# Kernel optimization log

Measured on AMD Instinct MI355X. Metric: run time of the kernel, lower is better.

The kernel has to match this reference:

```python
import jax, jax.numpy as jnp
import numpy as np

B, T, DIM, HEADS = 4, 2048, 1024, 16
D_K = DIM // HEADS


def setup_inputs() -> dict:
    key = jax.random.key(0)
    ks = jax.random.split(key, 5)
    x = jax.random.normal(ks[0], (B, T, DIM), dtype=jnp.float32)
    # nn.Linear params: weight [out, in], bias [out]
    w_qkv = jax.random.normal(ks[1], (3 * DIM, DIM), dtype=jnp.float32) / np.sqrt(DIM)
    b_qkv = jax.random.normal(ks[2], (3 * DIM,), dtype=jnp.float32) * 0.02
    w_out = jax.random.normal(ks[3], (DIM, DIM), dtype=jnp.float32) / np.sqrt(DIM)
    b_out = jax.random.normal(ks[4], (DIM,), dtype=jnp.float32) * 0.02
    # causal mask, broadcast over batch and heads: [1, 1, T, T]
    mask = jnp.tril(jnp.ones((T, T), dtype=jnp.int32))[None, None]
    return {"x": x, "w_qkv": w_qkv, "b_qkv": b_qkv, "w_out": w_out, "b_out": b_out, "mask": mask}


def reference(x, w_qkv, b_qkv, w_out, b_out, mask):
    Bb, Tt, D = x.shape
    # fused QKV projection: [B,T,3D] -> [3,B,H,T,d_k]
    qkv = (x @ w_qkv.T + b_qkv).reshape(Bb, Tt, 3, HEADS, D_K).transpose(2, 0, 3, 1, 4)
    q, k, v = qkv[0], qkv[1], qkv[2]
    scores = jnp.einsum("bhqd,bhkd->bhqk", q, k) / jnp.sqrt(jnp.float32(D_K))
    scores = jnp.where(mask == 0, -jnp.inf, scores)
    attn = jax.nn.softmax(scores, axis=-1)  # [B,H,T,T]
    context = jnp.einsum("bhqk,bhkd->bhqd", attn, v)
    context = context.transpose(0, 2, 1, 3).reshape(Bb, Tt, D)
    return context @ w_out.T + b_out
```

## Files before the change

kernel.cpp:

```cpp
#include <hip/hip_runtime.h>

typedef unsigned short ushort_t;
typedef __bf16 bf16x8 __attribute__((ext_vector_type(8)));
typedef float f32x4 __attribute__((ext_vector_type(4)));

#define BB 4
#define TT 2048
#define DIMD 1024
#define NH 16
#define DK 64
#define MROWS (BB * TT)
#define NQKV (3 * DIMD)

__device__ __forceinline__ ushort_t f2b(float f) {
  __bf16 h = (__bf16)f;
  union { __bf16 h; ushort_t u; } c; c.h = h; return c.u;
}
__device__ __forceinline__ float fexp2(float x) {
  float r;
  asm("v_exp_f32 %0, %1" : "=v"(r) : "v"(x));
  return r;
}

__device__ __forceinline__ void gload_lds16(const void* g, void* l) {
  __builtin_amdgcn_global_load_lds(
      (const __attribute__((address_space(1))) void*)g,
      (__attribute__((address_space(3))) void*)l,
      16, 0, 0);
}

__global__ __launch_bounds__(256) void cast_f32_bf16(
    const float* __restrict__ in, ushort_t* __restrict__ out, int n)
{
  const int i = (blockIdx.x * 256 + threadIdx.x) * 8;
  if (i >= n) return;
  float4 a = *(const float4*)(in + i);
  float4 b = *(const float4*)(in + i + 4);
  ushort_t o[8];
  o[0] = f2b(a.x); o[1] = f2b(a.y); o[2] = f2b(a.z); o[3] = f2b(a.w);
  o[4] = f2b(b.x); o[5] = f2b(b.y); o[6] = f2b(b.z); o[7] = f2b(b.w);
  *(uint4*)(out + i) = *(const uint4*)o;
}

template <bool OUT_F32>
__global__ __launch_bounds__(512, 4) void gemm_bt_pipe(
    const ushort_t* __restrict__ A, const ushort_t* __restrict__ W,
    const float* __restrict__ bias, void* __restrict__ Cp,
    int M, int N, int K)
{
  __shared__ __align__(16) ushort_t As[3][128 * 32];
  __shared__ __align__(16) ushort_t Bs[3][256 * 32];

  const int tid = threadIdx.x;
  const int wave = tid >> 6, lane = tid & 63;
  const int x = blockIdx.x & 7, j = blockIdx.x >> 3;
  const int bm = (x << 3) | (j & 7);
  const int bn = j >> 3;
  const int row0 = bm << 7, col0 = bn << 8;
  const int wm = (wave >> 2) << 6;
  const int wn = (wave & 3) << 6;
  const int fr = lane & 15;
  const int g  = lane >> 4;
  const int g4 = g << 2;
  const int csw = (g ^ (fr >> 2)) << 3;

  const int srow = lane >> 2;
  const int scol = ((lane & 3) ^ ((lane >> 4) & 3)) << 3;
  const int lbase = wave << 9;

  const ushort_t* Ag  = A + (size_t)(row0 + (wave << 4) + srow) * K + scol;
  const ushort_t* Wg0 = W + (size_t)(col0 + (wave << 4) + srow) * K + scol;
  const ushort_t* Wg1 = Wg0 + (size_t)128 * K;

#define STAGE_P(kt, buf)                                                      \
  {                                                                           \
    const size_t _k = (size_t)(kt) << 5;                                      \
    gload_lds16(Ag + _k,  &As[buf][lbase]);                                   \
    gload_lds16(Wg0 + _k, &Bs[buf][lbase]);                                   \
    gload_lds16(Wg1 + _k, &Bs[buf][4096 + lbase]);                            \
  }

  const int NT = K >> 5;
  STAGE_P(0, 0);
  STAGE_P(1, 1);

  f32x4 acc[4][4] = {};
  int cr = 0, st = 2;

  for (int t = 0; t < NT; ++t) {
    if (t + 1 < NT) asm volatile("s_waitcnt vmcnt(3)" ::: "memory");
    else            asm volatile("s_waitcnt vmcnt(0)" ::: "memory");
    __builtin_amdgcn_s_barrier();

    const ushort_t* as_ = As[cr];
    const ushort_t* bs_ = Bs[cr];
    bf16x8 af0 = *(const bf16x8*)&as_[(wm +      fr) * 32 + csw];
    bf16x8 af1 = *(const bf16x8*)&as_[(wm + 16 + fr) * 32 + csw];
    bf16x8 bw0 = *(const bf16x8*)&bs_[(wn +      fr) * 32 + csw];
    bf16x8 bw1 = *(const bf16x8*)&bs_[(wn + 16 + fr) * 32 + csw];
    bf16x8 bw2 = *(const bf16x8*)&bs_[(wn + 32 + fr) * 32 + csw];
    bf16x8 bw3 = *(const bf16x8*)&bs_[(wn + 48 + fr) * 32 + csw];
    if (t + 2 < NT) STAGE_P(t + 2, st);
    asm volatile("s_waitcnt lgkmcnt(0)" ::: "memory");
    __builtin_amdgcn_sched_barrier(0);
    __builtin_amdgcn_s_setprio(1);
    acc[0][0] = __builtin_amdgcn_mfma_f32_16x16x32_bf16(af0, bw0, acc[0][0], 0, 0, 0);
    acc[0][1] = __builtin_amdgcn_mfma_f32_16x16x32_bf16(af0, bw1, acc[0][1], 0, 0, 0);
    acc[0][2] = __builtin_amdgcn_mfma_f32_16x16x32_bf16(af0, bw2, acc[0][2], 0, 0, 0);
    acc[0][3] = __builtin_amdgcn_mfma_f32_16x16x32_bf16(af0, bw3, acc[0][3], 0, 0, 0);
    acc[1][0] = __builtin_amdgcn_mfma_f32_16x16x32_bf16(af1, bw0, acc[1][0], 0, 0, 0);
    acc[1][1] = __builtin_amdgcn_mfma_f32_16x16x32_bf16(af1, bw1, acc[1][1], 0, 0, 0);
    acc[1][2] = __builtin_amdgcn_mfma_f32_16x16x32_bf16(af1, bw2, acc[1][2], 0, 0, 0);
    acc[1][3] = __builtin_amdgcn_mfma_f32_16x16x32_bf16(af1, bw3, acc[1][3], 0, 0, 0);
    __builtin_amdgcn_s_setprio(0);

    bf16x8 af2 = *(const bf16x8*)&as_[(wm + 32 + fr) * 32 + csw];
    bf16x8 af3 = *(const bf16x8*)&as_[(wm + 48 + fr) * 32 + csw];
    asm volatile("s_waitcnt lgkmcnt(0)" ::: "memory");
    __builtin_amdgcn_sched_barrier(0);
    __builtin_amdgcn_s_setprio(1);
    acc[2][0] = __builtin_amdgcn_mfma_f32_16x16x32_bf16(af2, bw0, acc[2][0], 0, 0, 0);
    acc[2][1] = __builtin_amdgcn_mfma_f32_16x16x32_bf16(af2, bw1, acc[2][1], 0, 0, 0);
    acc[2][2] = __builtin_amdgcn_mfma_f32_16x16x32_bf16(af2, bw2, acc[2][2], 0, 0, 0);
    acc[2][3] = __builtin_amdgcn_mfma_f32_16x16x32_bf16(af2, bw3, acc[2][3], 0, 0, 0);
    acc[3][0] = __builtin_amdgcn_mfma_f32_16x16x32_bf16(af3, bw0, acc[3][0], 0, 0, 0);
    acc[3][1] = __builtin_amdgcn_mfma_f32_16x16x32_bf16(af3, bw1, acc[3][1], 0, 0, 0);
    acc[3][2] = __builtin_amdgcn_mfma_f32_16x16x32_bf16(af3, bw2, acc[3][2], 0, 0, 0);
    acc[3][3] = __builtin_amdgcn_mfma_f32_16x16x32_bf16(af3, bw3, acc[3][3], 0, 0, 0);
    __builtin_amdgcn_s_setprio(0);

    ++cr; if (cr == 3) cr = 0;
    ++st; if (st == 3) st = 0;
  }
#undef STAGE_P

#pragma unroll
  for (int jj = 0; jj < 4; ++jj) {
    const int col = col0 + wn + (jj << 4) + fr;
    const float bv = bias[col];
#pragma unroll
    for (int i = 0; i < 4; ++i)
#pragma unroll
      for (int r = 0; r < 4; ++r) {
        const size_t row = (size_t)(row0 + wm + (i << 4) + g4 + r);
        if constexpr (OUT_F32)
          ((float*)Cp)[row * (size_t)N + col] = acc[i][jj][r] + bv;
        else
          ((ushort_t*)Cp)[row * (size_t)N + col] = f2b(acc[i][jj][r] + bv);
      }
  }
}

template <bool OUT_F32>
__global__ __launch_bounds__(256) void gemm_bt_bias(
    const ushort_t* __restrict__ A, const ushort_t* __restrict__ W,
    const float* __restrict__ bias, void* __restrict__ Cp,
    int M, int N, int K)
{
  __shared__ __align__(16) ushort_t As[128 * 32];
  __shared__ __align__(16) ushort_t Bs[128 * 32];

  const int tid = threadIdx.x;
  const int wave = tid >> 6, lane = tid & 63;
  const int tiles_n = N >> 7;
  const int bm = blockIdx.x / tiles_n, bn = blockIdx.x % tiles_n;
  const int row0 = bm << 7, col0 = bn << 7;
  const int wm = (wave >> 1) << 6;
  const int wn = (wave & 1) << 6;
  const int fr = lane & 15;
  const int fk = (lane >> 4) << 3;
  const int g4 = (lane >> 4) << 2;

  const int sr = lane >> 2;
  const int csw = fk ^ (((fr >> 1) & 3) << 3);

  f32x4 acc[4][4] = {};

  for (int k0 = 0; k0 < K; k0 += 32) {
    __syncthreads();
#pragma unroll
    for (int p = 0; p < 2; ++p) {
      const int e = (wave << 9) + (p << 11);
      const int r = (e >> 5) + sr;
      const int c = ((lane & 3) << 3) ^ (((r >> 1) & 3) << 3);
      gload_lds16(A + (size_t)(row0 + r) * K + (k0 + c), As + e);
      gload_lds16(W + (size_t)(col0 + r) * K + (k0 + c), Bs + e);
    }
    __syncthreads();

    bf16x8 af[4], bw[4];
#pragma unroll
    for (int i = 0; i < 4; ++i) {
      af[i] = *(const bf16x8*)&As[(wm + (i << 4) + fr) * 32 + csw];
      bw[i] = *(const bf16x8*)&Bs[(wn + (i << 4) + fr) * 32 + csw];
    }
#pragma unroll
    for (int mi = 0; mi < 4; ++mi)
#pragma unroll
      for (int ni = 0; ni < 4; ++ni)
        acc[mi][ni] = __builtin_amdgcn_mfma_f32_16x16x32_bf16(af[mi], bw[ni], acc[mi][ni], 0, 0, 0);
  }

#pragma unroll
  for (int ni = 0; ni < 4; ++ni) {
    const int col = col0 + wn + (ni << 4) + fr;
    const float bv = bias[col];
#pragma unroll
    for (int mi = 0; mi < 4; ++mi)
#pragma unroll
      for (int r = 0; r < 4; ++r) {
        const size_t row = (size_t)(row0 + wm + (mi << 4) + g4 + r);
        if constexpr (OUT_F32)
          ((float*)Cp)[row * (size_t)N + col] = acc[mi][ni][r] + bv;
        else
          ((ushort_t*)Cp)[row * (size_t)N + col] = f2b(acc[mi][ni][r] + bv);
      }
  }
}

#define C1 0.18033688011112042f
__global__ __launch_bounds__(256, 4) void attn_fused(
    const ushort_t* __restrict__ qkv, ushort_t* __restrict__ ctx)
{
  __shared__ __align__(16) ushort_t Ks[2][64 * 64];
  __shared__ __align__(16) ushort_t U[8192];
  ushort_t* const Vt = U;
  ushort_t* const Ps = U + 4096;
  ushort_t* const Qs = U;

  const int tid = threadIdx.x, wave = tid >> 6, lane = tid & 63;
  const int fr = lane & 15;
  const int g  = lane >> 4;
  const int fk = g << 3;
  const int g4 = g << 2;

  const int bid = blockIdx.x;
  const int bq  = (bid >> 3) & 15;
  const int G   = (bid & 7) | ((bid >> 7) << 3);
  const int h   = G & 15;
  const int b   = G >> 4;

  const int srl = lane >> 3;
  const int scc = ((lane & 7) ^ srl) << 3;
  const int vr  = tid >> 2;
  const int vc  = (tid & 3) << 4;
  const int rsw = (fr & 7) << 3;

  const ushort_t* Kg = qkv + (size_t)b * TT * NQKV + DIMD + h * DK;
  const ushort_t* Vg = qkv + (size_t)b * TT * NQKV + 2 * DIMD + h * DK;

#pragma unroll 1
  for (int t = 0; t < 2; ++t) {
    const int qt = t ? (31 - bq) : bq;
    const int ktmax = qt;
    const size_t qrow0 = (size_t)b * TT + (size_t)qt * 64;

    __syncthreads();

    const ushort_t* Qg = qkv + qrow0 * NQKV + h * DK;
    uint4 va = *(const uint4*)(Vg + (size_t)vr * NQKV + vc);
    uint4 vb = *(const uint4*)(Vg + (size_t)vr * NQKV + vc + 8);
#pragma unroll
    for (int p = 0; p < 2; ++p) {
      const int e  = (wave << 10) + (p << 9);
      const int rr = (e >> 6) + srl;
      gload_lds16(Qg + (size_t)rr * NQKV + scc, Qs + e);
      gload_lds16(Kg + (size_t)rr * NQKV + scc, Ks[0] + e);
    }
    asm volatile("s_waitcnt vmcnt(0)" ::: "memory");
    __syncthreads();

    bf16x8 aqr[2];
#pragma unroll
    for (int ks = 0; ks < 2; ++ks)
      aqr[ks] = *(const bf16x8*)&Qs[((wave << 4) + fr) * 64 + (((ks << 5) + fk) ^ rsw)];
    __syncthreads();

    const int qrow = (qt << 6) + (wave << 4) + fr;
    float mrow = -1e30f, lrow = 0.f;
    f32x4 oacc[4] = {};
    int cur = 0;

    for (int kt = 0; kt <= ktmax; ++kt) {
      {
        __align__(16) ushort_t tmp[16];
        *(uint4*)&tmp[0] = va;
        *(uint4*)&tmp[8] = vb;
#pragma unroll
        for (int jj = 0; jj < 16; ++jj) {
          const int d  = vc + jj;
          const int hh = (d & 7) ^ ((d >> 3) & 7);
          Vt[d * 64 + (vr ^ (hh << 3))] = tmp[jj];
        }
      }
      if (kt < ktmax) {
        const size_t krow = (size_t)(kt + 1) << 6;
#pragma unroll
        for (int p = 0; p < 2; ++p) {
          const int e  = (wave << 10) + (p << 9);
          const int rr = (e >> 6) + srl;
          gload_lds16(Kg + (krow + rr) * NQKV + scc, Ks[cur ^ 1] + e);
        }
        va = *(const uint4*)(Vg + (krow + vr) * NQKV + vc);
        vb = *(const uint4*)(Vg + (krow + vr) * NQKV + vc + 8);
      }
      asm volatile("s_waitcnt lgkmcnt(0)" ::: "memory");
      __builtin_amdgcn_s_barrier();

      f32x4 s[4] = {};
      __builtin_amdgcn_s_setprio(1);
#pragma unroll
      for (int ks = 0; ks < 2; ++ks)
#pragma unroll
        for (int ni = 0; ni < 4; ++ni) {
          const bf16x8 bk = *(const bf16x8*)&Ks[cur][((ni << 4) + fr) * 64 + (((ks << 5) + fk) ^ rsw)];
          s[ni] = __builtin_amdgcn_mfma_f32_16x16x32_bf16(bk, aqr[ks], s[ni], 0, 0, 0);
        }
      __builtin_amdgcn_s_setprio(0);

      if (kt == ktmax) {
        const int kb = kt << 6;
#pragma unroll
        for (int ni = 0; ni < 4; ++ni)
#pragma unroll
          for (int r = 0; r < 4; ++r) {
            const int kc = kb + (ni << 4) + g4 + r;
            if (kc > qrow) s[ni][r] = -1e30f;
          }
      }

      float rm = -1e30f;
#pragma unroll
      for (int ni = 0; ni < 4; ++ni) {
        const float m01 = fmaxf(s[ni][0], s[ni][1]);
        const float m23 = fmaxf(s[ni][2], s[ni][3]);
        rm = fmaxf(rm, fmaxf(m01, m23));
      }
      rm = fmaxf(rm, __shfl_xor(rm, 16, 64));
      rm = fmaxf(rm, __shfl_xor(rm, 32, 64));

      if (__any(rm > mrow + 64.f)) {
        const float mn = fmaxf(mrow, rm);
        const float corr = fexp2((mrow - mn) * C1);
        mrow = mn;
        lrow *= corr;
#pragma unroll
        for (int ni = 0; ni < 4; ++ni) oacc[ni] *= corr;
      }
      const float nm2 = -mrow * C1;
      float rs = 0.f;
#pragma unroll
      for (int ni = 0; ni < 4; ++ni)
#pragma unroll
        for (int r = 0; r < 4; ++r) {
          const float pe = fexp2(fmaf(s[ni][r], C1, nm2));
          s[ni][r] = pe;
          rs += pe;
        }
      rs += __shfl_xor(rs, 16, 64);
      rs += __shfl_xor(rs, 32, 64);
      lrow += rs;

#pragma unroll
      for (int ni = 0; ni < 4; ++ni) {
        ushort_t o4[4];
#pragma unroll
        for (int r = 0; r < 4; ++r) o4[r] = f2b(s[ni][r]);
        *(uint2*)&Ps[(wave << 10) + fr * 64 + (((ni << 4) + g4) ^ rsw)] = *(const uint2*)o4;
      }
      asm volatile("s_waitcnt lgkmcnt(0)" ::: "memory");
      __builtin_amdgcn_sched_barrier(0);

      __builtin_amdgcn_s_setprio(1);
#pragma unroll
      for (int ks = 0; ks < 2; ++ks) {
        const bf16x8 ap = *(const bf16x8*)&Ps[(wave << 10) + fr * 64 + (((ks << 5) + fk) ^ rsw)];
#pragma unroll
        for (int ni = 0; ni < 4; ++ni) {
          const int hh = (fr & 7) ^ ((2 * ni + (fr >> 3)) & 7);
          const bf16x8 bv = *(const bf16x8*)&Vt[((ni << 4) + fr) * 64 + (((ks << 5) + fk) ^ (hh << 3))];
          oacc[ni] = __builtin_amdgcn_mfma_f32_16x16x32_bf16(bv, ap, oacc[ni], 0, 0, 0);
        }
      }
      __builtin_amdgcn_s_setprio(0);

      if (kt < ktmax) {
        asm volatile("s_waitcnt vmcnt(0)" ::: "memory");
        __syncthreads();
      }
      cur ^= 1;
    }

    const float inv = 1.f / lrow;
    ushort_t* crow = ctx + (qrow0 + (wave << 4) + fr) * DIMD + h * DK;
#pragma unroll
    for (int ni = 0; ni < 4; ++ni) {
      ushort_t o4[4];
#pragma unroll
      for (int r = 0; r < 4; ++r) o4[r] = f2b(oacc[ni][r] * inv);
      *(uint2*)&crow[(ni << 4) + g4] = *(const uint2*)o4;
    }
  }
}

extern "C" void kernel_launch(void* const* d_in, const int* in_sizes, int n_in,
                              void* d_out, int out_size, void* d_ws, size_t ws_size,
                              hipStream_t stream) {
  const float* x     = (const float*)d_in[0];
  const float* w_qkv = (const float*)d_in[1];
  const float* b_qkv = (const float*)d_in[2];
  const float* w_out = (const float*)d_in[3];
  const float* b_out = (const float*)d_in[4];

  const size_t need = 36u * 1024 * 1024 * sizeof(ushort_t);
  if (ws_size < need) return;

  ushort_t* qkv = (ushort_t*)d_ws;
  ushort_t* xb  = qkv + (size_t)MROWS * NQKV;
  ushort_t* wqb = xb  + (size_t)MROWS * DIMD;
  ushort_t* wob = wqb + (size_t)NQKV * DIMD;
  ushort_t* ctx = xb;
  float*    out = (float*)d_out;

  cast_f32_bf16<<<dim3(MROWS * DIMD / 2048), dim3(256), 0, stream>>>(x, xb, MROWS * DIMD);
  cast_f32_bf16<<<dim3(NQKV * DIMD / 2048), dim3(256), 0, stream>>>(w_qkv, wqb, NQKV * DIMD);
  cast_f32_bf16<<<dim3(DIMD * DIMD / 2048), dim3(256), 0, stream>>>(w_out, wob, DIMD * DIMD);
  gemm_bt_pipe<false><<<dim3((MROWS / 128) * (NQKV / 256)), dim3(512), 0, stream>>>(
      xb, wqb, b_qkv, (void*)qkv, MROWS, NQKV, DIMD);
  attn_fused<<<dim3(BB * NH * 16), dim3(256), 0, stream>>>(qkv, ctx);
  gemm_bt_bias<true><<<dim3((MROWS / 128) * (DIMD / 128)), dim3(256), 0, stream>>>(
      ctx, wob, b_out, (void*)out, MROWS, DIMD, DIMD);
}
```

Before: 186.9 us.

## Process paired causal query tiles concurrently to share K/V tile loads

Before, each block handled two query tiles (bq and 31-bq) one after the other, loading K and V tiles for each pass. Now both query tiles are processed in a single sweep over the key tiles, so every K/V tile loaded into LDS serves both queries. The short tile only runs while kt <= qa. This cuts K/V global traffic and barrier count roughly in half and gives more MFMA work between syncs. In exchange it uses more registers for the two sets of accumulators and softmax state, plus 8 KB more LDS for a second P buffer, which may lower occupancy below the launch bound of 4.

Result: slower. 383.8 us (+105.3%).

```diff
diff --git a/kernel.cpp b/kernel.cpp
--- a/kernel.cpp
+++ b/kernel.cpp
@@ -223,10 +223,11 @@
     const ushort_t* __restrict__ qkv, ushort_t* __restrict__ ctx)
 {
   __shared__ __align__(16) ushort_t Ks[2][64 * 64];
-  __shared__ __align__(16) ushort_t U[8192];
-  ushort_t* const Vt = U;
-  ushort_t* const Ps = U + 4096;
-  ushort_t* const Qs = U;
+  __shared__ __align__(16) ushort_t U[12288];
+  ushort_t* const Vt  = U;
+  ushort_t* const PsB = U + 4096;
+  ushort_t* const PsA = U + 8192;
+  ushort_t* const Qs  = U;
 
   const int tid = threadIdx.x, wave = tid >> 6, lane = tid & 63;
   const int fr = lane & 15;
@@ -246,158 +247,222 @@
   const int vc  = (tid & 3) << 4;
   const int rsw = (fr & 7) << 3;
 
+  const int qa = bq, qb = 31 - bq;
+
   const ushort_t* Kg = qkv + (size_t)b * TT * NQKV + DIMD + h * DK;
   const ushort_t* Vg = qkv + (size_t)b * TT * NQKV + 2 * DIMD + h * DK;
-
-#pragma unroll 1
-  for (int t = 0; t < 2; ++t) {
-    const int qt = t ? (31 - bq) : bq;
-    const int ktmax = qt;
-    const size_t qrow0 = (size_t)b * TT + (size_t)qt * 64;
-
-    __syncthreads();
-
-    const ushort_t* Qg = qkv + qrow0 * NQKV + h * DK;
-    uint4 va = *(const uint4*)(Vg + (size_t)vr * NQKV + vc);
-    uint4 vb = *(const uint4*)(Vg + (size_t)vr * NQKV + vc + 8);
-#pragma unroll
-    for (int p = 0; p < 2; ++p) {
-      const int e  = (wave << 10) + (p << 9);
-      const int rr = (e >> 6) + srl;
-      gload_lds16(Qg + (size_t)rr * NQKV + scc, Qs + e);
-      gload_lds16(Kg + (size_t)rr * NQKV + scc, Ks[0] + e);
-    }
-    asm volatile("s_waitcnt vmcnt(0)" ::: "memory");
-    __syncthreads();
-
-    bf16x8 aqr[2];
+  const size_t qrow0A = (size_t)b * TT + (size_t)qa * 64;
+  const size_t qrow0B = (size_t)b * TT + (size_t)qb * 64;
+
+  uint4 va = *(const uint4*)(Vg + (size_t)vr * NQKV + vc);
+  uint4 vb = *(const uint4*)(Vg + (size_t)vr * NQKV + vc + 8);
+  const ushort_t* QgA = qkv + qrow0A * NQKV + h * DK;
+  const ushort_t* QgB = qkv + qrow0B * NQKV + h * DK;
+#pragma unroll
+  for (int p = 0; p < 2; ++p) {
+    const int e  = (wave << 10) + (p << 9);
+    const int rr = (wave << 4) + (p << 3) + srl;
+    gload_lds16(QgA + (size_t)rr * NQKV + scc, Qs + e);
+    gload_lds16(QgB + (size_t)rr * NQKV + scc, Qs + 4096 + e);
+    gload_lds16(Kg  + (size_t)rr * NQKV + scc, Ks[0] + e);
+  }
+  asm volatile("s_waitcnt vmcnt(0)" ::: "memory");
+  __syncthreads();
+
+  bf16x8 aqrA[2], aqrB[2];
+#pragma unroll
+  for (int ks = 0; ks < 2; ++ks) {
+    aqrA[ks] = *(const bf16x8*)&Qs[((wave << 4) + fr) * 64 + (((ks << 5) + fk) ^ rsw)];
+    aqrB[ks] = *(const bf16x8*)&Qs[4096 + ((wave << 4) + fr) * 64 + (((ks << 5) + fk) ^ rsw)];
+  }
+  __syncthreads();
+
+  const int qrowA = (qa << 6) + (wave << 4) + fr;
+  const int qrowB = (qb << 6) + (wave << 4) + fr;
+  float mA = -1e30f, lA = 0.f, mB = -1e30f, lB = 0.f;
+  f32x4 oA[4] = {}, oB[4] = {};
+  int cur = 0;
+
+  for (int kt = 0; kt <= qb; ++kt) {
+    {
+      __align__(16) ushort_t tmp[16];
+      *(uint4*)&tmp[0] = va;
+      *(uint4*)&tmp[8] = vb;
+#pragma unroll
+      for (int jj = 0; jj < 16; ++jj) {
+        const int d  = vc + jj;
+        const int hh = (d & 7) ^ ((d >> 3) & 7);
+        Vt[d * 64 + (vr ^ (hh << 3))] = tmp[jj];
+      }
+    }
+    if (kt < qb) {
+      const size_t krow = (size_t)(kt + 1) << 6;
+#pragma unroll
+      for (int p = 0; p < 2; ++p) {
+        const int e  = (wave << 10) + (p << 9);
+        const int rr = (wave << 4) + (p << 3) + srl;
+        gload_lds16(Kg + (krow + rr) * NQKV + scc, Ks[cur ^ 1] + e);
+      }
+      va = *(const uint4*)(Vg + (krow + vr) * NQKV + vc);
+      vb = *(const uint4*)(Vg + (krow + vr) * NQKV + vc + 8);
+    }
+    asm volatile("s_waitcnt lgkmcnt(0)" ::: "memory");
+    __builtin_amdgcn_s_barrier();
+
+    const bool doA = (kt <= qa);
+
+    f32x4 sA[4] = {}, sB[4] = {};
+    __builtin_amdgcn_s_setprio(1);
 #pragma unroll
     for (int ks = 0; ks < 2; ++ks)
-      aqr[ks] = *(const bf16x8*)&Qs[((wave << 4) + fr) * 64 + (((ks << 5) + fk) ^ rsw)];
-    __syncthreads();
-
-    const int qrow = (qt << 6) + (wave << 4) + fr;
-    float mrow = -1e30f, lrow = 0.f;
-    f32x4 oacc[4] = {};
-    int cur = 0;
-
-    for (int kt = 0; kt <= ktmax; ++kt) {
-      {
-        __align__(16) ushort_t tmp[16];
-        *(uint4*)&tmp[0] = va;
-        *(uint4*)&tmp[8] = vb;
-#pragma unroll
-        for (int jj = 0; jj < 16; ++jj) {
-          const int d  = vc + jj;
-          const int hh = (d & 7) ^ ((d >> 3) & 7);
-          Vt[d * 64 + (vr ^ (hh << 3))] = tmp[jj];
-        }
-      }
-      if (kt < ktmax) {
-        const size_t krow = (size_t)(kt + 1) << 6;
-#pragma unroll
-        for (int p = 0; p < 2; ++p) {
-          const int e  = (wave << 10) + (p << 9);
-          const int rr = (e >> 6) + srl;
-          gload_lds16(Kg + (krow + rr) * NQKV + scc, Ks[cur ^ 1] + e);
-        }
-        va = *(const uint4*)(Vg + (krow + vr) * NQKV + vc);
-        vb = *(const uint4*)(Vg + (krow + vr) * NQKV + vc + 8);
-      }
-      asm volatile("s_waitcnt lgkmcnt(0)" ::: "memory");
-      __builtin_amdgcn_s_barrier();
-
-      f32x4 s[4] = {};
-      __builtin_amdgcn_s_setprio(1);
-#pragma unroll
-      for (int ks = 0; ks < 2; ++ks)
-#pragma unroll
-        for (int ni = 0; ni < 4; ++ni) {
-          const bf16x8 bk = *(const bf16x8*)&Ks[cur][((ni << 4) + fr) * 64 + (((ks << 5) + fk) ^ rsw)];
-          s[ni] = __builtin_amdgcn_mfma_f32_16x16x32_bf16(bk, aqr[ks], s[ni], 0, 0, 0);
-        }
-      __builtin_amdgcn_s_setprio(0);
-
-      if (kt == ktmax) {
+#pragma unroll
+      for (int ni = 0; ni < 4; ++ni) {
+        const bf16x8 bk = *(const bf16x8*)&Ks[cur][((ni << 4) + fr) * 64 + (((ks << 5) + fk) ^ rsw)];
+        sB[ni] = __builtin_amdgcn_mfma_f32_16x16x32_bf16(bk, aqrB[ks], sB[ni], 0, 0, 0);
+        if (doA)
+          sA[ni] = __builtin_amdgcn_mfma_f32_16x16x32_bf16(bk, aqrA[ks], sA[ni], 0, 0, 0);
+      }
+    __builtin_amdgcn_s_setprio(0);
+
+    {
+      if (kt == qb) {
         const int kb = kt << 6;
 #pragma unroll
         for (int ni = 0; ni < 4; ++ni)
 #pragma unroll
           for (int r = 0; r < 4; ++r) {
             const int kc = kb + (ni << 4) + g4 + r;
-            if (kc > qrow) s[ni][r] = -1e30f;
+            if (kc > qrowB) sB[ni][r] = -1e30f;
           }
       }
-
       float rm = -1e30f;
 #pragma unroll
-      for (int ni = 0; ni < 4; ++ni) {
-        const float m01 = fmaxf(s[ni][0], s[ni][1]);
-        const float m23 = fmaxf(s[ni][2], s[ni][3]);
-        rm = fmaxf(rm, fmaxf(m01, m23));
-      }
+      for (int ni = 0; ni < 4; ++ni)
+        rm = fmaxf(rm, fmaxf(fmaxf(sB[ni][0], sB[ni][1]), fmaxf(sB[ni][2], sB[ni][3])));
       rm = fmaxf(rm, __shfl_xor(rm, 16, 64));
       rm = fmaxf(rm, __shfl_xor(rm, 32, 64));
-
-      if (__any(rm > mrow + 64.f)) {
-        const float mn = fmaxf(mrow, rm);
-        const float corr = fexp2((mrow - mn) * C1);
-        mrow = mn;
-        lrow *= corr;
-#pragma unroll
-        for (int ni = 0; ni < 4; ++ni) oacc[ni] *= corr;
-      }
-      const float nm2 = -mrow * C1;
+      if (__any(rm > mB + 64.f)) {
+        const float mn = fmaxf(mB, rm);
+        const float corr = fexp2((mB - mn) * C1);
+        mB = mn; lB *= corr;
+#pragma unroll
+        for (int ni = 0; ni < 4; ++ni) oB[ni] *= corr;
+      }
+      const float nm2 = -mB * C1;
       float rs = 0.f;
 #pragma unroll
       for (int ni = 0; ni < 4; ++ni)
 #pragma unroll
         for (int r = 0; r < 4; ++r) {
-          const float pe = fexp2(fmaf(s[ni][r], C1, nm2));
-          s[ni][r] = pe;
+          const float pe = fexp2(fmaf(sB[ni][r], C1, nm2));
+          sB[ni][r] = pe;
           rs += pe;
         }
       rs += __shfl_xor(rs, 16, 64);
       rs += __shfl_xor(rs, 32, 64);
-      lrow += rs;
-
+      lB += rs;
 #pragma unroll
       for (int ni = 0; ni < 4; ++ni) {
         ushort_t o4[4];
 #pragma unroll
-        for (int r = 0; r < 4; ++r) o4[r] = f2b(s[ni][r]);
-        *(uint2*)&Ps[(wave << 10) + fr * 64 + (((ni << 4) + g4) ^ rsw)] = *(const uint2*)o4;
-      }
-      asm volatile("s_waitcnt lgkmcnt(0)" ::: "memory");
-      __builtin_amdgcn_sched_barrier(0);
-
-      __builtin_amdgcn_s_setprio(1);
-#pragma unroll
-      for (int ks = 0; ks < 2; ++ks) {
-        const bf16x8 ap = *(const bf16x8*)&Ps[(wave << 10) + fr * 64 + (((ks << 5) + fk) ^ rsw)];
-#pragma unroll
-        for (int ni = 0; ni < 4; ++ni) {
-          const int hh = (fr & 7) ^ ((2 * ni + (fr >> 3)) & 7);
-          const bf16x8 bv = *(const bf16x8*)&Vt[((ni << 4) + fr) * 64 + (((ks << 5) + fk) ^ (hh << 3))];
-          oacc[ni] = __builtin_amdgcn_mfma_f32_16x16x32_bf16(bv, ap, oacc[ni], 0, 0, 0);
+        for (int r = 0; r < 4; ++r) o4[r] = f2b(sB[ni][r]);
+        *(uint2*)&PsB[(wave << 10) + fr * 64 + (((ni << 4) + g4) ^ rsw)] = *(const uint2*)o4;
+      }
+    }
+
+    if (doA) {
+      if (kt == qa) {
+        const int kb = kt << 6;
+#pragma unroll
+        for (int ni = 0; ni < 4; ++ni)
+#pragma unroll
+          for (int r = 0; r < 4; ++r) {
+            const int kc = kb + (ni << 4) + g4 + r;
+            if (kc > qrowA) sA[ni][r] = -1e30f;
+          }
+      }
+      float rm = -1e30f;
+#pragma unroll
+      for (int ni = 0; ni < 4; ++ni)
+        rm = fmaxf(rm, fmaxf(fmaxf(sA[ni][0], sA[ni][1]), fmaxf(sA[ni][2], sA[ni][3])));
+      rm = fmaxf(rm, __shfl_xor(rm, 16, 64));
+      rm = fmaxf(rm, __shfl_xor(rm, 32, 64));
+      if (__any(rm > mA + 64.f)) {
+        const float mn = fmaxf(mA, rm);
+        const float corr = fexp2((mA - mn) * C1);
+        mA = mn; lA *= corr;
+#pragma unroll
+        for (int ni = 0; ni < 4; ++ni) oA[ni] *= corr;
+      }
+      const float nm2 = -mA * C1;
+      float rs = 0.f;
+#pragma unroll
+      for (int ni = 0; ni < 4; ++ni)
+#pragma unroll
+        for (int r = 0; r < 4; ++r) {
+          const float pe = fexp2(fmaf(sA[ni][r], C1, nm2));
+          sA[ni][r] = pe;
+          rs += pe;
         }
-      }
-      __builtin_amdgcn_s_setprio(0);
-
-      if (kt < ktmax) {
-        asm volatile("s_waitcnt vmcnt(0)" ::: "memory");
-        __syncthreads();
-      }
-      cur ^= 1;
-    }
-
-    const float inv = 1.f / lrow;
-    ushort_t* crow = ctx + (qrow0 + (wave << 4) + fr) * DIMD + h * DK;
+      rs += __shfl_xor(rs, 16, 64);
+      rs += __shfl_xor(rs, 32, 64);
+      lA += rs;
+#pragma unroll
+      for (int ni = 0; ni < 4; ++ni) {
+        ushort_t o4[4];
+#pragma unroll
+        for (int r = 0; r < 4; ++r) o4[r] = f2b(sA[ni][r]);
+        *(uint2*)&PsA[(wave << 10) + fr * 64 + (((ni << 4) + g4) ^ rsw)] = *(const uint2*)o4;
+      }
+    }
+
+    asm volatile("s_waitcnt lgkmcnt(0)" ::: "memory");
+    __builtin_amdgcn_sched_barrier(0);
+
+    __builtin_amdgcn_s_setprio(1);
+#pragma unroll
+    for (int ks = 0; ks < 2; ++ks) {
+      const bf16x8 apB = *(const bf16x8*)&PsB[(wave << 10) + fr * 64 + (((ks << 5) + fk) ^ rsw)];
+      bf16x8 apA{};
+      if (doA)
+        apA = *(const bf16x8*)&PsA[(wave << 10) + fr * 64 + (((ks << 5) + fk) ^ rsw)];
+#pragma unroll
+      for (int ni = 0; ni < 4; ++ni) {
+        const int hh = (fr & 7) ^ ((2 * ni + (fr >> 3)) & 7);
+        const bf16x8 bv = *(const bf16x8*)&Vt[((ni << 4) + fr) * 64 + (((ks << 5) + fk) ^ (hh << 3))];
+        oB[ni] = __builtin_amdgcn_mfma_f32_16x16x32_bf16(bv, apB, oB[ni], 0, 0, 0);
+        if (doA)
+          oA[ni] = __builtin_amdgcn_mfma_f32_16x16x32_bf16(bv, apA, oA[ni], 0, 0, 0);
+      }
+    }
+    __builtin_amdgcn_s_setprio(0);
+
+    if (kt < qb) {
+      asm volatile("s_waitcnt vmcnt(0)" ::: "memory");
+      __syncthreads();
+    }
+    cur ^= 1;
+  }
+
+  {
+    const float inv = 1.f / lB;
+    ushort_t* crow = ctx + (qrow0B + (wave << 4) + fr) * DIMD + h * DK;
 #pragma unroll
     for (int ni = 0; ni < 4; ++ni) {
       ushort_t o4[4];
 #pragma unroll
-      for (int r = 0; r < 4; ++r) o4[r] = f2b(oacc[ni][r] * inv);
+      for (int r = 0; r < 4; ++r) o4[r] = f2b(oB[ni][r] * inv);
+      *(uint2*)&crow[(ni << 4) + g4] = *(const uint2*)o4;
+    }
+  }
+  {
+    const float inv = 1.f / lA;
+    ushort_t* crow = ctx + (qrow0A + (wave << 4) + fr) * DIMD + h * DK;
+#pragma unroll
+    for (int ni = 0; ni < 4; ++ni) {
+      ushort_t o4[4];
+#pragma unroll
+      for (int r = 0; r < 4; ++r) o4[r] = f2b(oA[ni][r] * inv);
       *(uint2*)&crow[(ni << 4) + g4] = *(const uint2*)o4;
     }
   }
```
